# Kernel optimization log

Hardware: AMD Instinct MI355X
Metric: run time of the kernel (lower is better)

The kernel has to match this reference:

```python
import jax, jax.numpy as jnp
import numpy as np

N_NODES = 140000   # 14 frames * 10000 nodes/frame
N_EDGES = 2240000  # avg degree 16
NFEAT = 128
NHID = 128
N_FRAMES = 14


def setup_inputs() -> dict:
    key = jax.random.key(0)
    k1, k2, k3, k4, k5 = jax.random.split(key, 5)
    x = jax.random.normal(k1, (N_NODES, NFEAT), dtype=jnp.float32)
    # gc1 parameters (only layer actually used in forward)
    W = jax.random.normal(k2, (NFEAT, NHID), dtype=jnp.float32) * 0.05
    b = jnp.zeros((NHID,), dtype=jnp.float32)
    # sparse normalized adjacency as COO edge list (row sorted for fast segment_sum)
    edge_row = jnp.sort(jax.random.randint(k3, (N_EDGES,), 0, N_NODES, dtype=jnp.int32))
    edge_col = jax.random.randint(k4, (N_EDGES,), 0, N_NODES, dtype=jnp.int32)
    edge_val = jax.random.uniform(k5, (N_EDGES,), dtype=jnp.float32)
    return {"x": x, "W": W, "b": b, "edge_val": edge_val,
            "edge_row": edge_row, "edge_col": edge_col}


def reference(x, W, b, edge_val, edge_row, edge_col):
    # GraphConvolution: adj @ (x @ W) + b  (adj sparse, COO)
    support = x @ W                                   # [N, NHID]
    msgs = edge_val[:, None] * support[edge_col]      # [E, NHID] gather
    agg = jax.ops.segment_sum(msgs, edge_row, num_segments=N_NODES,
                              indices_are_sorted=True)  # [N, NHID] scatter-add
    h = jax.nn.relu(agg + b)
    # view(14, -1, c) then max over frame axis
    h = h.reshape(N_FRAMES, -1, NHID)                 # [14, N/14, NHID]
    h = jnp.max(h, axis=0)                            # [N/14, NHID]
    return jax.nn.log_softmax(h, axis=1)
```

## Files before the change

kernel.cpp:

```cpp
#include <hip/hip_runtime.h>
#include <hip/hip_bf16.h>

#define N_NODES 140000
#define N_EDGES 2240000
#define NFEAT 128
#define NHID 128
#define N_FRAMES 14
#define NODES_PER_FRAME 10000
#define CAP 224

typedef __attribute__((ext_vector_type(8))) short frag_b16;
typedef __attribute__((ext_vector_type(4))) int frag_i4;
typedef __attribute__((ext_vector_type(4))) float f32x4;

__device__ __forceinline__ unsigned short f2bf(float f) {
    union { float f; unsigned int u; } v; v.f = f;
    unsigned int r = v.u + 0x7fffu + ((v.u >> 16) & 1u);
    return (unsigned short)(r >> 16);
}
__device__ __forceinline__ int pk_bf16(float a, float b) {
    union { __hip_bfloat162 h; int i; } u;
    u.h = __float22bfloat162_rn(make_float2(a, b));
    return u.i;
}
__device__ __forceinline__ float2 bf2x2(unsigned int u) {
    union { unsigned int u; float f; } lo, hi;
    lo.u = u << 16;
    hi.u = u & 0xffff0000u;
    return make_float2(lo.f, hi.f);
}

__global__ void convert_wt(const float* __restrict__ W, unsigned short* __restrict__ WT) {
    int idx = blockIdx.x * blockDim.x + threadIdx.x;
    if (idx >= NFEAT * NHID) return;
    int k = idx >> 7, n = idx & 127;
    WT[n * 128 + k] = f2bf(W[idx]);
}

__global__ void build_row_ptr(const int* __restrict__ edge_row, int* __restrict__ row_ptr) {
    int e = blockIdx.x * blockDim.x + threadIdx.x;
    if (e >= N_EDGES) return;
    int r = edge_row[e];
    int prev = (e == 0) ? -1 : edge_row[e - 1];
    for (int q = prev + 1; q <= r; ++q) row_ptr[q] = e;
    if (e == N_EDGES - 1) {
        for (int q = r + 1; q <= N_NODES; ++q) row_ptr[q] = N_EDGES;
    }
}

#define WT_STRIDE 136

__global__ __launch_bounds__(256) void gemm_kernel(
        const float* __restrict__ x, const unsigned short* __restrict__ WT,
        unsigned short* __restrict__ support) {
    __shared__ unsigned short wt_lds[128 * WT_STRIDE];

    const uint4* WTv = (const uint4*)WT;
    for (int idx = threadIdx.x; idx < 2048; idx += 256) {
        uint4 d = WTv[idx];
        int elem = idx << 3;
        int n = elem >> 7, k = elem & 127;
        *(uint4*)&wt_lds[n * WT_STRIDE + k] = d;
    }

    int wave = threadIdx.x >> 6;
    int lane = threadIdx.x & 63;
    int m = lane & 15;
    int q = lane >> 4;

    long row0 = (long)blockIdx.x * 64 + wave * 16;

    int arow = (int)row0 + m;
    if (arow >= N_NODES) arow = N_NODES - 1;
    const float* xrow = x + (long)arow * 128 + q * 8;
    frag_b16 xa[4];
#pragma unroll
    for (int ks = 0; ks < 4; ++ks) {
        float4 lo = *(const float4*)(xrow + ks * 32);
        float4 hi = *(const float4*)(xrow + ks * 32 + 4);
        union { frag_b16 f; frag_i4 i; } u;
        u.i[0] = pk_bf16(lo.x, lo.y);
        u.i[1] = pk_bf16(lo.z, lo.w);
        u.i[2] = pk_bf16(hi.x, hi.y);
        u.i[3] = pk_bf16(hi.z, hi.w);
        xa[ks] = u.f;
    }

    __syncthreads();

    if (row0 < N_NODES) {
        f32x4 acc[8];
#pragma unroll
        for (int t = 0; t < 8; ++t) acc[t] = (f32x4){0.f, 0.f, 0.f, 0.f};

#pragma unroll
        for (int t = 0; t < 8; ++t) {
            const unsigned short* bp = &wt_lds[(t * 16 + m) * WT_STRIDE + q * 8];
#pragma unroll
            for (int ks = 0; ks < 4; ++ks) {
                frag_b16 wfrag = *(const frag_b16*)(bp + ks * 32);
                acc[t] = __builtin_amdgcn_mfma_f32_16x16x32_bf16(wfrag, xa[ks], acc[t], 0, 0, 0);
            }
        }

        long node = row0 + m;
        if (node < N_NODES) {
            unsigned short* srow = support + node * 128;
#pragma unroll
            for (int t = 0; t < 8; ++t) {
                int2 pk;
                pk.x = pk_bf16(acc[t][0], acc[t][1]);
                pk.y = pk_bf16(acc[t][2], acc[t][3]);
                *(int2*)(srow + t * 16 + q * 4) = pk;
            }
        }
    }
}

__global__ __launch_bounds__(128) void agg_kernel(
        const unsigned short* __restrict__ support, const float* __restrict__ b,
        const float* __restrict__ edge_val, const int* __restrict__ edge_col,
        const int* __restrict__ row_ptr, float* __restrict__ out) {
    __shared__ int   segStart[2][8];
    __shared__ int   segOff[2][8];
    __shared__ int   eCol[2][CAP];
    __shared__ float eVal[2][CAP];
    __shared__ float xch[2][64][2];

    const int i = blockIdx.x;
    const int lane = threadIdx.x & 63;
    const int w = threadIdx.x >> 6;
    const unsigned int* sup32 = (const unsigned int*)support;

    int a = 0, len = 0;
    if (lane < 7) {
        int n = (w * 7 + lane) * NODES_PER_FRAME + i;
        a = row_ptr[n];
        len = row_ptr[n + 1] - a;
    }
    int off = 0;
#pragma unroll
    for (int f2 = 0; f2 < 7; ++f2) {
        int L2 = __shfl(len, f2);
        if (f2 < lane) off += L2;
    }
    if (lane < 7) { segStart[w][lane] = a; segOff[w][lane] = off; }
    if (lane == 6) segOff[w][7] = off + len;
    __syncthreads();

#pragma unroll 1
    for (int f = 0; f < 7; ++f) {
        int g = segStart[w][f], s = segOff[w][f], L = segOff[w][f + 1] - s;
        for (int j = lane; j < L; j += 64) {
            int d = s + j;
            if (d < CAP) { eCol[w][d] = edge_col[g + j]; eVal[w][d] = edge_val[g + j]; }
        }
    }
    __syncthreads();

    const float2 bb = *(const float2*)&b[lane * 2];
    float2 mx = make_float2(0.f, 0.f);

#pragma unroll 1
    for (int f = 0; f < 7; ++f) {
        int g = segStart[w][f], s = segOff[w][f], L = segOff[w][f + 1] - s;
        float ax = 0.f, ay = 0.f;
        int j = 0;
        for (; j + 8 <= L; j += 8) {
            int cols[8]; float vals[8];
#pragma unroll
            for (int u = 0; u < 8; ++u) {
                int d = s + j + u;
                if (d < CAP) { cols[u] = eCol[w][d]; vals[u] = eVal[w][d]; }
                else         { cols[u] = edge_col[g + j + u]; vals[u] = edge_val[g + j + u]; }
            }
            unsigned int sv[8];
#pragma unroll
            for (int u = 0; u < 8; ++u) sv[u] = sup32[(cols[u] << 6) | lane];
#pragma unroll
            for (int u = 0; u < 8; ++u) {
                float2 s2 = bf2x2(sv[u]);
                ax = fmaf(vals[u], s2.x, ax);
                ay = fmaf(vals[u], s2.y, ay);
            }
        }
        for (; j < L; ++j) {
            int d = s + j; int c; float v;
            if (d < CAP) { c = eCol[w][d]; v = eVal[w][d]; }
            else         { c = edge_col[g + j]; v = edge_val[g + j]; }
            float2 s2 = bf2x2(sup32[(c << 6) | lane]);
            ax = fmaf(v, s2.x, ax);
            ay = fmaf(v, s2.y, ay);
        }
        float hx = ax + bb.x, hy = ay + bb.y;
        mx.x = fmaxf(mx.x, hx > 0.f ? hx : 0.f);
        mx.y = fmaxf(mx.y, hy > 0.f ? hy : 0.f);
    }

    xch[w][lane][0] = mx.x;
    xch[w][lane][1] = mx.y;
    __syncthreads();
    float ox = fmaxf(xch[0][lane][0], xch[1][lane][0]);
    float oy = fmaxf(xch[0][lane][1], xch[1][lane][1]);

    float M = fmaxf(ox, oy);
#pragma unroll
    for (int o = 32; o >= 1; o >>= 1) M = fmaxf(M, __shfl_xor(M, o));
    float S = __expf(ox - M) + __expf(oy - M);
#pragma unroll
    for (int o = 32; o >= 1; o >>= 1) S += __shfl_xor(S, o);

    if (w == 0) {
        float ls = __logf(S);
        float2 o2 = make_float2((ox - M) - ls, (oy - M) - ls);
        *(float2*)&out[i * 128 + lane * 2] = o2;
    }
}

extern "C" void kernel_launch(void* const* d_in, const int* in_sizes, int n_in,
                              void* d_out, int out_size, void* d_ws, size_t ws_size,
                              hipStream_t stream) {
    const float* x        = (const float*)d_in[0];
    const float* W        = (const float*)d_in[1];
    const float* b        = (const float*)d_in[2];
    const float* edge_val = (const float*)d_in[3];
    const int*   edge_row = (const int*)d_in[4];
    const int*   edge_col = (const int*)d_in[5];
    float* out = (float*)d_out;

    char* ws = (char*)d_ws;
    unsigned short* support = (unsigned short*)ws;
    unsigned short* WT      = (unsigned short*)(ws + 35840000);
    int*            row_ptr = (int*)(ws + 35840000 + 32768);

    convert_wt<<<64, 256, 0, stream>>>(W, WT);
    build_row_ptr<<<(N_EDGES + 255) / 256, 256, 0, stream>>>(edge_row, row_ptr);
    gemm_kernel<<<(N_NODES + 63) / 64, 256, 0, stream>>>(x, WT, support);
    agg_kernel<<<NODES_PER_FRAME, 128, 0, stream>>>(support, b, edge_val, edge_col, row_ptr, out);
}
```

Baseline: 244.5 us.

## Pad edge segments to multiples of 8 in LDS and merge prep kernels

Merges the weight-transpose and row_ptr build kernels into a single launch. In the aggregation kernel, edge column and value are packed into an int2 LDS buffer, and each frame segment is zero-padded to a multiple of 8 so the inner gather loop has no scalar tail and no per-element CAP check. CAP is raised to 352, and a simple global-memory fallback path handles waves whose edges do not fit. The padded entries gather from row 0 with zero weight, which adds some wasted loads, and the larger LDS buffer may reduce occupancy.

```diff
diff --git a/kernel.cpp b/kernel.cpp
--- a/kernel.cpp
+++ b/kernel.cpp
@@ -7,7 +7,7 @@
 #define NHID 128
 #define N_FRAMES 14
 #define NODES_PER_FRAME 10000
-#define CAP 224
+#define CAP 352
 
 typedef __attribute__((ext_vector_type(8))) short frag_b16;
 typedef __attribute__((ext_vector_type(4))) int frag_i4;
@@ -30,21 +30,20 @@
     return make_float2(lo.f, hi.f);
 }
 
-__global__ void convert_wt(const float* __restrict__ W, unsigned short* __restrict__ WT) {
-    int idx = blockIdx.x * blockDim.x + threadIdx.x;
-    if (idx >= NFEAT * NHID) return;
-    int k = idx >> 7, n = idx & 127;
-    WT[n * 128 + k] = f2bf(W[idx]);
-}
-
-__global__ void build_row_ptr(const int* __restrict__ edge_row, int* __restrict__ row_ptr) {
+__global__ void prep_kernel(const float* __restrict__ W, unsigned short* __restrict__ WT,
+                            const int* __restrict__ edge_row, int* __restrict__ row_ptr) {
     int e = blockIdx.x * blockDim.x + threadIdx.x;
-    if (e >= N_EDGES) return;
-    int r = edge_row[e];
-    int prev = (e == 0) ? -1 : edge_row[e - 1];
-    for (int q = prev + 1; q <= r; ++q) row_ptr[q] = e;
-    if (e == N_EDGES - 1) {
-        for (int q = r + 1; q <= N_NODES; ++q) row_ptr[q] = N_EDGES;
+    if (e < NFEAT * NHID) {
+        int k = e >> 7, n = e & 127;
+        WT[n * 128 + k] = f2bf(W[e]);
+    }
+    if (e < N_EDGES) {
+        int r = edge_row[e];
+        int prev = (e == 0) ? -1 : edge_row[e - 1];
+        for (int q = prev + 1; q <= r; ++q) row_ptr[q] = e;
+        if (e == N_EDGES - 1) {
+            for (int q = r + 1; q <= N_NODES; ++q) row_ptr[q] = N_EDGES;
+        }
     }
 }
 
@@ -122,15 +121,16 @@
         const float* __restrict__ edge_val, const int* __restrict__ edge_col,
         const int* __restrict__ row_ptr, float* __restrict__ out) {
     __shared__ int   segStart[2][8];
+    __shared__ int   segLen[2][8];
     __shared__ int   segOff[2][8];
-    __shared__ int   eCol[2][CAP];
-    __shared__ float eVal[2][CAP];
+    __shared__ int2  eBuf[2][CAP];
     __shared__ float xch[2][64][2];
 
     const int i = blockIdx.x;
     const int lane = threadIdx.x & 63;
     const int w = threadIdx.x >> 6;
-    const unsigned int* sup32 = (const unsigned int*)support;
+    const char* supB = (const char*)support;
+    const unsigned lane4 = (unsigned)lane * 4u;
 
     int a = 0, len = 0;
     if (lane < 7) {
@@ -138,22 +138,30 @@
         a = row_ptr[n];
         len = row_ptr[n + 1] - a;
     }
+    int len8 = (len + 7) & ~7;
     int off = 0;
 #pragma unroll
     for (int f2 = 0; f2 < 7; ++f2) {
-        int L2 = __shfl(len, f2);
+        int L2 = __shfl(len8, f2);
         if (f2 < lane) off += L2;
     }
-    if (lane < 7) { segStart[w][lane] = a; segOff[w][lane] = off; }
-    if (lane == 6) segOff[w][7] = off + len;
-    __syncthreads();
-
+    if (lane < 7) { segStart[w][lane] = a; segLen[w][lane] = len; segOff[w][lane] = off; }
+    if (lane == 6) segOff[w][7] = off + len8;
+    __syncthreads();
+
+    const bool fit = segOff[w][7] <= CAP;
+
+    if (fit) {
 #pragma unroll 1
-    for (int f = 0; f < 7; ++f) {
-        int g = segStart[w][f], s = segOff[w][f], L = segOff[w][f + 1] - s;
-        for (int j = lane; j < L; j += 64) {
-            int d = s + j;
-            if (d < CAP) { eCol[w][d] = edge_col[g + j]; eVal[w][d] = edge_val[g + j]; }
+        for (int f = 0; f < 7; ++f) {
+            int g = segStart[w][f], s = segOff[w][f], L = segLen[w][f];
+            int L8 = (L + 7) & ~7;
+            for (int j = lane; j < L8; j += 64) {
+                int2 v;
+                if (j < L) { v.x = edge_col[g + j]; v.y = __float_as_int(edge_val[g + j]); }
+                else       { v.x = 0; v.y = 0; }
+                eBuf[w][s + j] = v;
+            }
         }
     }
     __syncthreads();
@@ -161,40 +169,49 @@
     const float2 bb = *(const float2*)&b[lane * 2];
     float2 mx = make_float2(0.f, 0.f);
 
+    if (fit) {
 #pragma unroll 1
-    for (int f = 0; f < 7; ++f) {
-        int g = segStart[w][f], s = segOff[w][f], L = segOff[w][f + 1] - s;
-        float ax = 0.f, ay = 0.f;
-        int j = 0;
-        for (; j + 8 <= L; j += 8) {
-            int cols[8]; float vals[8];
-#pragma unroll
-            for (int u = 0; u < 8; ++u) {
-                int d = s + j + u;
-                if (d < CAP) { cols[u] = eCol[w][d]; vals[u] = eVal[w][d]; }
-                else         { cols[u] = edge_col[g + j + u]; vals[u] = edge_val[g + j + u]; }
-            }
-            unsigned int sv[8];
-#pragma unroll
-            for (int u = 0; u < 8; ++u) sv[u] = sup32[(cols[u] << 6) | lane];
-#pragma unroll
-            for (int u = 0; u < 8; ++u) {
-                float2 s2 = bf2x2(sv[u]);
-                ax = fmaf(vals[u], s2.x, ax);
-                ay = fmaf(vals[u], s2.y, ay);
-            }
-        }
-        for (; j < L; ++j) {
-            int d = s + j; int c; float v;
-            if (d < CAP) { c = eCol[w][d]; v = eVal[w][d]; }
-            else         { c = edge_col[g + j]; v = edge_val[g + j]; }
-            float2 s2 = bf2x2(sup32[(c << 6) | lane]);
-            ax = fmaf(v, s2.x, ax);
-            ay = fmaf(v, s2.y, ay);
-        }
-        float hx = ax + bb.x, hy = ay + bb.y;
-        mx.x = fmaxf(mx.x, hx > 0.f ? hx : 0.f);
-        mx.y = fmaxf(mx.y, hy > 0.f ? hy : 0.f);
+        for (int f = 0; f < 7; ++f) {
+            int s = segOff[w][f];
+            int e8 = s + ((segLen[w][f] + 7) & ~7);
+            float ax = 0.f, ay = 0.f;
+            for (int j = s; j < e8; j += 8) {
+                unsigned sv[8];
+                float vv[8];
+#pragma unroll
+                for (int u = 0; u < 8; ++u) {
+                    int2 ed = eBuf[w][j + u];
+                    unsigned o = ((unsigned)ed.x << 8) + lane4;
+                    sv[u] = *(const unsigned*)(supB + o);
+                    vv[u] = __int_as_float(ed.y);
+                }
+#pragma unroll
+                for (int u = 0; u < 8; ++u) {
+                    float2 s2 = bf2x2(sv[u]);
+                    ax = fmaf(vv[u], s2.x, ax);
+                    ay = fmaf(vv[u], s2.y, ay);
+                }
+            }
+            float hx = ax + bb.x, hy = ay + bb.y;
+            mx.x = fmaxf(mx.x, hx > 0.f ? hx : 0.f);
+            mx.y = fmaxf(mx.y, hy > 0.f ? hy : 0.f);
+        }
+    } else {
+#pragma unroll 1
+        for (int f = 0; f < 7; ++f) {
+            int g = segStart[w][f], L = segLen[w][f];
+            float ax = 0.f, ay = 0.f;
+            for (int j = 0; j < L; ++j) {
+                int c = edge_col[g + j];
+                float v = edge_val[g + j];
+                float2 s2 = bf2x2(*(const unsigned*)(supB + (((unsigned)c << 8) + lane4)));
+                ax = fmaf(v, s2.x, ax);
+                ay = fmaf(v, s2.y, ay);
+            }
+            float hx = ax + bb.x, hy = ay + bb.y;
+            mx.x = fmaxf(mx.x, hx > 0.f ? hx : 0.f);
+            mx.y = fmaxf(mx.y, hy > 0.f ? hy : 0.f);
+        }
     }
 
     xch[w][lane][0] = mx.x;
@@ -233,8 +250,7 @@
     unsigned short* WT      = (unsigned short*)(ws + 35840000);
     int*            row_ptr = (int*)(ws + 35840000 + 32768);
 
-    convert_wt<<<64, 256, 0, stream>>>(W, WT);
-    build_row_ptr<<<(N_EDGES + 255) / 256, 256, 0, stream>>>(edge_row, row_ptr);
+    prep_kernel<<<(N_EDGES + 255) / 256, 256, 0, stream>>>(W, WT, edge_row, row_ptr);
     gemm_kernel<<<(N_NODES + 63) / 64, 256, 0, stream>>>(x, WT, support);
     agg_kernel<<<NODES_PER_FRAME, 128, 0, stream>>>(support, b, edge_val, edge_col, row_ptr, out);
 }
```

New measurement: 221.4 us. -9.4%, faster.
